# Kernel tuning notes

Measured on AMD Instinct MI355X. Metric: run time of the kernel, lower is better.

Reference implementation:

```python
import jax, jax.numpy as jnp
import numpy as np

B, MAXN, D, H, S = 64, 512, 512, 8, 32
DH = D // H          # per-head dim = 64
N = B * MAXN         # 32768 total nodes
E = 524288           # ~avg degree 16
EPS = 1e-5


def setup_inputs() -> dict:
    key = jax.random.key(0)
    ks = jax.random.split(key, 18)
    s = 0.05
    x_dense = jax.random.normal(ks[0], (B, MAXN, D), jnp.float32)
    x = jax.random.normal(ks[1], (N, D), jnp.float32)
    src = jax.random.randint(ks[2], (E,), 0, N)
    # destinations kept within the same graph as the source
    dst = (src // MAXN) * MAXN + jax.random.randint(ks[3], (E,), 0, MAXN)
    edge_index = jnp.stack([src, dst]).astype(jnp.int32)
    batch = (jnp.arange(N) // MAXN).astype(jnp.int32)  # sorted, 512 nodes/graph
    seed = jax.random.normal(ks[4], (S, 1, D), jnp.float32) * s
    # per-head GCN conv weights concatenated along output dim: [D, H*DH] == [D, D]
    Wk = jax.random.normal(ks[5], (D, D), jnp.float32) * s
    bk = jnp.zeros((D,), jnp.float32)
    Wv = jax.random.normal(ks[6], (D, D), jnp.float32) * s
    bv = jnp.zeros((D,), jnp.float32)
    q_proj_weight = jax.random.normal(ks[7], (D, D), jnp.float32) * s
    Wo = jax.random.normal(ks[8], (D, D), jnp.float32) * s
    bo = jnp.zeros((D,), jnp.float32)
    Wff = jax.random.normal(ks[9], (D, D), jnp.float32) * s
    bff = jnp.zeros((D,), jnp.float32)
    gamma_h = jnp.ones((D,), jnp.float32)
    beta_h = jnp.zeros((D,), jnp.float32)
    gamma_z = jnp.ones((D,), jnp.float32)
    beta_z = jnp.zeros((D,), jnp.float32)
    return dict(x_dense=x_dense, x=x, edge_index=edge_index, batch=batch,
                seed=seed, Wk=Wk, bk=bk, Wv=Wv, bv=bv,
                q_proj_weight=q_proj_weight, Wo=Wo, bo=bo, Wff=Wff, bff=bff,
                gamma_h=gamma_h, beta_h=beta_h, gamma_z=gamma_z, beta_z=beta_z)


def _gcn(x, W, b, src, dst):
    # PyG GCNConv with self-loops + symmetric norm; all H heads fused via W [D, H*DH]
    xw = x @ W                                   # [N, D]
    idx = jnp.arange(N)
    src_f = jnp.concatenate([src, idx])
    dst_f = jnp.concatenate([dst, idx])
    deg = jax.ops.segment_sum(jnp.ones_like(dst_f, dtype=x.dtype), dst_f, num_segments=N)
    dinv = jax.lax.rsqrt(deg)                    # deg >= 1 (self-loops)
    norm = dinv[src_f] * dinv[dst_f]             # [E+N]
    out = jax.ops.segment_sum(xw[src_f] * norm[:, None], dst_f, num_segments=N)
    return out + b


def _to_dense(feat, batch):
    # to_dense_batch for sorted batch vector; padded slots are zeros
    counts = jax.ops.segment_sum(jnp.ones((N,), jnp.int32), batch, num_segments=B)
    start = jnp.cumsum(counts) - counts
    pos = jnp.arange(N) - start[batch]
    return jnp.zeros((B, MAXN, feat.shape[-1]), feat.dtype).at[batch, pos].set(feat)


def _layernorm(x, g, b):
    m = jnp.mean(x, -1, keepdims=True)
    v = jnp.mean(jnp.square(x - m), -1, keepdims=True)
    return (x - m) * jax.lax.rsqrt(v + EPS) * g + b


def reference(x_dense, x, edge_index, batch, seed, Wk, bk, Wv, bv,
              q_proj_weight, Wo, bo, Wff, bff, gamma_h, beta_h, gamma_z, beta_z):
    src, dst = edge_index[0], edge_index[1]
    k_nodes = _gcn(x, Wk, bk, src, dst)          # [N, D] (H heads concat)
    v_nodes = _gcn(x, Wv, bv, src, dst)
    k_dense = _to_dense(k_nodes, batch)          # [B, MAXN, D]
    v_dense = _to_dense(v_nodes, batch)

    # query: seed [S,1,D] repeated over batch -> [S,B,D]; q projection (F.linear)
    query = jnp.broadcast_to(seed, (S, B, D))
    q = jnp.einsum('sbd,ed->sbe', query, q_proj_weight)
    scale = 1.0 / jnp.sqrt(jnp.float32(DH))
    qh = (q * scale).reshape(S, B, H, DH).transpose(1, 2, 0, 3)     # [B,H,S,DH]
    kh = k_dense.reshape(B, MAXN, H, DH).transpose(0, 2, 1, 3)      # [B,H,N,DH]
    vh = v_dense.reshape(B, MAXN, H, DH).transpose(0, 2, 1, 3)
    scores = jnp.einsum('bhsd,bhnd->bhsn', qh, kh)                  # [B,H,S,MAXN]
    attn = jax.nn.softmax(scores, axis=-1)                          # no padding mask (faithful)
    ctx = jnp.einsum('bhsn,bhnd->bhsd', attn, vh)                   # [B,H,S,DH]
    ctx = ctx.transpose(0, 2, 1, 3).reshape(B, S, D)                # heads concat
    attn_out = ctx @ Wo.T + bo                                      # [B,S,D]

    query_bse = jnp.broadcast_to(seed.transpose(1, 0, 2), (B, S, D))
    embed = _layernorm(query_bse + attn_out, gamma_h, beta_h)
    embed = _layernorm(embed + embed @ Wff.T + bff, gamma_z, beta_z)
    return embed
```

## Files before the change

kernel.cpp:

```cpp
#include <hip/hip_runtime.h>
#include <hip/hip_bf16.h>

#define BN   64
#define MAXN 512
#define DIM  512
#define NH   8
#define NS   32
#define NN   32768
#define NE   524288
#define MP   (2048 * 512)

typedef __hip_bfloat16 bf16;
using bf16x8 = __attribute__((ext_vector_type(8))) short;
using f32x4  = __attribute__((ext_vector_type(4))) float;

__device__ int   g_cnt[NN];
__device__ int   g_cur[NN];
__device__ int   g_off[NN + 1];
__device__ int   g_csr[NE];
__device__ float g_dinv[NN];
__device__ bf16  g_xb[NN * DIM];
__device__ bf16  g_agg[NN * DIM];
__device__ bf16  g_aggT[NN * DIM];
__device__ bf16  g_qf[256 * DIM];
__device__ bf16  g_wob[DIM * DIM];
__device__ bf16  g_wvb[DIM * DIM];
__device__ bf16  g_wvo[DIM * 8 * DIM];
__device__ float g_bvo[DIM];
__device__ bf16  g_wffT[DIM * DIM];
__device__ float g_q[NS * DIM];
__device__ bf16  g_sc[BN * 256 * MAXN];
__device__ bf16  g_cp[BN * NS * 8 * DIM];
__device__ float g_part[4 * MP];
__device__ float g_h1[BN * NS * DIM];
__device__ bf16  g_h1b[BN * NS * DIM];

__device__ inline float bf2f(unsigned short u) {
    union { unsigned int i; float f; } x; x.i = ((unsigned int)u) << 16; return x.f;
}

__device__ inline void gll16(const bf16* g, bf16* l) {
    __builtin_amdgcn_global_load_lds(
        (const __attribute__((address_space(1))) void*)g,
        (__attribute__((address_space(3))) void*)l, 16, 0, 0);
}

__global__ void k_zero() {
    int i = blockIdx.x * 256 + threadIdx.x;
    if (i < NN) { g_cnt[i] = 0; g_cur[i] = 0; }
}

__global__ __launch_bounds__(256) void k_cntprep(const int* __restrict__ dst,
                                                 const float* __restrict__ seed,
                                                 const float* __restrict__ Wq,
                                                 const float* __restrict__ Wo,
                                                 const float* __restrict__ Wv,
                                                 const float* __restrict__ Wff,
                                                 const float* __restrict__ bo,
                                                 const float* __restrict__ bv) {
    int blk = blockIdx.x;
    if (blk < 2048) {
        int e = blk * 256 + threadIdx.x;
        atomicAdd(&g_cnt[dst[e]], 1);
    } else if (blk < 2112) {
        int i = (blk - 2048) * 256 + threadIdx.x;
        int s = i >> 9, e = i & 511;
        const float* sr = seed + s * DIM;
        const float* wr = Wq + e * DIM;
        float a0 = 0.f, a1 = 0.f;
        for (int d = 0; d < DIM; d += 8) {
            float4 a = *(const float4*)(sr + d);
            float4 b = *(const float4*)(wr + d);
            float4 c = *(const float4*)(sr + d + 4);
            float4 w = *(const float4*)(wr + d + 4);
            a0 += a.x * b.x + a.y * b.y + a.z * b.z + a.w * b.w;
            a1 += c.x * w.x + c.y * w.y + c.z * w.z + c.w * w.w;
        }
        g_q[i] = (a0 + a1) * 0.125f;
    } else if (blk < 2496) {
        long t = (long)(blk - 2112) * 256 + threadIdx.x;
        const float* src; bf16* dstp; long off;
        if (t < 32768)      { src = Wo;  dstp = g_wob;  off = t; }
        else if (t < 65536) { src = Wv;  dstp = g_wvb;  off = t - 32768; }
        else                { src = Wff; dstp = g_wffT; off = t - 65536; }
        long i = off * 8;
        float4 a = *(const float4*)(src + i);
        float4 b = *(const float4*)(src + i + 4);
        float v[8] = {a.x, a.y, a.z, a.w, b.x, b.y, b.z, b.w};
        bf16x8 o;
#pragma unroll
        for (int j = 0; j < 8; j++) { bf16 q = __float2bfloat16(v[j]); o[j] = *(short*)&q; }
        *(bf16x8*)(dstp + i) = o;
    } else {
        int e = (blk - 2496) * 256 + threadIdx.x;
        const float* orow = Wo + (long)e * DIM;
        float a0 = 0.f, a1 = 0.f;
        for (int c = 0; c < DIM; c += 8) {
            float4 a = *(const float4*)(bv + c);
            float4 w = *(const float4*)(orow + c);
            float4 xx = *(const float4*)(bv + c + 4);
            float4 u = *(const float4*)(orow + c + 4);
            a0 += a.x * w.x + a.y * w.y + a.z * w.z + a.w * w.w;
            a1 += xx.x * u.x + xx.y * u.y + xx.z * u.z + xx.w * u.w;
        }
        g_bvo[e] = bo[e] + a0 + a1;
    }
}

__global__ void k_scan() {
    __shared__ int part[1024];
    int t = threadIdx.x;
    int base = t * 32;
    int loc[32]; int s = 0;
#pragma unroll
    for (int i = 0; i < 32; i++) { loc[i] = g_cnt[base + i]; s += loc[i]; }
    part[t] = s; __syncthreads();
    for (int o = 1; o < 1024; o <<= 1) {
        int v = (t >= o) ? part[t - o] : 0;
        __syncthreads();
        part[t] += v;
        __syncthreads();
    }
    int ex = (t == 0) ? 0 : part[t - 1];
#pragma unroll
    for (int i = 0; i < 32; i++) {
        g_off[base + i] = ex; ex += loc[i];
        g_dinv[base + i] = rsqrtf(1.0f + (float)loc[i]);
    }
    if (t == 1023) g_off[NN] = ex;
}

__device__ __forceinline__ void gemm128(const bf16* __restrict__ A, long lda,
                                        const bf16* __restrict__ Bt, long ldb,
                                        long row0, long col0, int kbeg, int kend,
                                        bf16 (*As)[128 * 32], bf16 (*Bs)[128 * 32],
                                        f32x4 acc[4][4]) {
    int tid = threadIdx.x;
    int lane = tid & 63, wave = tid >> 6;
    int wr = wave >> 1, wc = wave & 1;
    int fr = lane & 15, fq = lane >> 4;
    int rchunk = (fq ^ ((fr >> 1) & 3)) * 8;
    int u0 = wave * 128 + lane;
    int sr0 = u0 >> 2, sc0 = ((u0 & 3) ^ ((sr0 >> 1) & 3)) * 8;
    int u1 = u0 + 64;
    int sr1 = u1 >> 2, sc1 = ((u1 & 3) ^ ((sr1 >> 1) & 3)) * 8;

    auto stage = [&](int buf, int kt) {
        gll16(A + (row0 + sr0) * lda + kt + sc0, As[buf] + u0 * 8);
        gll16(A + (row0 + sr1) * lda + kt + sc1, As[buf] + u1 * 8);
        gll16(Bt + (col0 + sr0) * ldb + kt + sc0, Bs[buf] + u0 * 8);
        gll16(Bt + (col0 + sr1) * ldb + kt + sc1, Bs[buf] + u1 * 8);
    };

    stage(0, kbeg);
    __syncthreads();
    for (int kt = kbeg; kt < kend; kt += 32) {
        int buf = ((kt - kbeg) >> 5) & 1;
        if (kt + 32 < kend) stage(buf ^ 1, kt + 32);
        bf16x8 af[4], bfv[4];
#pragma unroll
        for (int mi = 0; mi < 4; mi++)
            af[mi] = *(const bf16x8*)(As[buf] + (wr * 64 + mi * 16 + fr) * 32 + rchunk);
#pragma unroll
        for (int ni = 0; ni < 4; ni++)
            bfv[ni] = *(const bf16x8*)(Bs[buf] + (wc * 64 + ni * 16 + fr) * 32 + rchunk);
#pragma unroll
        for (int mi = 0; mi < 4; mi++)
#pragma unroll
            for (int ni = 0; ni < 4; ni++)
                acc[mi][ni] = __builtin_amdgcn_mfma_f32_16x16x32_bf16(af[mi], bfv[ni], acc[mi][ni], 0, 0, 0);
        __syncthreads();
    }
}

#define ACC_INIT                                             \
    f32x4 acc[4][4];                                         \
    _Pragma("unroll")                                        \
    for (int i = 0; i < 4; i++)                              \
        _Pragma("unroll")                                    \
        for (int j = 0; j < 4; j++) acc[i][j] = (f32x4){0.f, 0.f, 0.f, 0.f}; \
    int lane = threadIdx.x & 63, wave = threadIdx.x >> 6;    \
    int wr = wave >> 1, wc = wave & 1;                       \
    int fr = lane & 15, fq = lane >> 4;

__global__ __launch_bounds__(256) void k_fillxb(const int* __restrict__ src,
                                                const int* __restrict__ dst,
                                                const float* __restrict__ x,
                                                const float* __restrict__ Wk) {
    __shared__ bf16 As[2][128 * 32];
    __shared__ bf16 Bs[2][128 * 32];
    int blk = blockIdx.x;
    if (blk < 2048) {
        int e = blk * 256 + threadIdx.x;
        int d = dst[e];
        int p = atomicAdd(&g_cur[d], 1);
        g_csr[g_off[d] + p] = src[e];
    } else if (blk < 10240) {
        long i = (long)(blk - 2048) * (256 * 8) + (long)threadIdx.x * 8;
        int node = (int)(i >> 9);
        float w = g_dinv[node];
        float4 a = *(const float4*)(x + i);
        float4 b = *(const float4*)(x + i + 4);
        float v[8] = {a.x, a.y, a.z, a.w, b.x, b.y, b.z, b.w};
        bf16x8 o;
#pragma unroll
        for (int j = 0; j < 8; j++) { bf16 t = __float2bfloat16(v[j] * w); o[j] = *(short*)&t; }
        *(bf16x8*)(g_xb + i) = o;
    } else if (blk < 10752) {
        int i = (blk - 10240) * 256 + threadIdx.x;
        int hs = i >> 9, d = i & 511;
        int h = hs >> 5, s = hs & 31;
        const float* qr = g_q + s * DIM + h * 64;
        const float* wr = Wk + d * DIM + h * 64;
        float a0 = 0.f, a1 = 0.f;
        for (int t2 = 0; t2 < 64; t2 += 8) {
            float4 a = *(const float4*)(qr + t2);
            float4 w = *(const float4*)(wr + t2);
            float4 c = *(const float4*)(qr + t2 + 4);
            float4 u = *(const float4*)(wr + t2 + 4);
            a0 += a.x * w.x + a.y * w.y + a.z * w.z + a.w * w.w;
            a1 += c.x * u.x + c.y * u.y + c.z * u.z + c.w * u.w;
        }
        g_qf[i] = __float2bfloat16(a0 + a1);
    } else {
        int wi = blk - 10752;
        int bx = wi & 3, by = (wi >> 2) & 3, h = wi >> 4;
        ACC_INIT
        long row0 = (long)bx * 128, col0 = (long)by * 128;
        gemm128(g_wob, DIM, g_wvb, DIM, row0, col0, h * 64, h * 64 + 64, As, Bs, acc);
#pragma unroll
        for (int mi = 0; mi < 4; mi++)
#pragma unroll
            for (int ni = 0; ni < 4; ni++) {
                long col = col0 + wc * 64 + ni * 16 + fr;
#pragma unroll
                for (int r = 0; r < 4; r++) {
                    long row = row0 + wr * 64 + mi * 16 + fq * 4 + r;
                    g_wvo[row * 4096 + h * 512 + col] = __float2bfloat16(acc[mi][ni][r]);
                }
            }
    }
}

__global__ __launch_bounds__(256) void k_gather() {
    int bid = blockIdx.x;
    int lb = (bid & 7) * 1024 + (bid >> 3);
    int wave = threadIdx.x >> 6, lane = threadIdx.x & 63;
    int node = lb * 4 + wave;

    bf16x8 sv = ((const bf16x8*)(g_xb + (long)node * DIM))[lane];
    float acc[8];
#pragma unroll
    for (int j = 0; j < 8; j++) acc[j] = bf2f((unsigned short)sv[j]);

    int e = g_off[node], e1 = g_off[node + 1];
    for (; e + 8 <= e1; e += 8) {
        bf16x8 r[8];
#pragma unroll
        for (int q = 0; q < 8; q++)
            r[q] = ((const bf16x8*)(g_xb + (long)g_csr[e + q] * DIM))[lane];
#pragma unroll
        for (int j = 0; j < 8; j++) {
            float s01 = bf2f((unsigned short)r[0][j]) + bf2f((unsigned short)r[1][j]);
            float s23 = bf2f((unsigned short)r[2][j]) + bf2f((unsigned short)r[3][j]);
            float s45 = bf2f((unsigned short)r[4][j]) + bf2f((unsigned short)r[5][j]);
            float s67 = bf2f((unsigned short)r[6][j]) + bf2f((unsigned short)r[7][j]);
            acc[j] += (s01 + s23) + (s45 + s67);
        }
    }
    for (; e < e1; e++) {
        bf16x8 r0 = ((const bf16x8*)(g_xb + (long)g_csr[e] * DIM))[lane];
#pragma unroll
        for (int j = 0; j < 8; j++) acc[j] += bf2f((unsigned short)r0[j]);
    }
    float dd = g_dinv[node];
    bf16x8 o;
#pragma unroll
    for (int j = 0; j < 8; j++) { bf16 t = __float2bfloat16(acc[j] * dd); o[j] = *(short*)&t; }
    ((bf16x8*)(g_agg + (long)node * DIM))[lane] = o;
}

__global__ __launch_bounds__(256) void k_aggsc() {
    __shared__ __align__(16) char smem[32768];
    int blk = blockIdx.x;
    if (blk < 512) {
        bf16 (*As)[128 * 32] = (bf16(*)[128 * 32])smem;
        bf16 (*Bs)[128 * 32] = (bf16(*)[128 * 32])(smem + 16384);
        int b = blk & 63, bx = (blk >> 6) & 1, by = blk >> 7;
        ACC_INIT
        long row0 = (long)bx * 128, col0 = (long)by * 128;
        gemm128(g_qf, DIM, g_agg + (long)b * (MAXN * DIM), DIM, row0, col0, 0, DIM, As, Bs, acc);
        bf16* out = g_sc + (long)b * (256 * MAXN);
#pragma unroll
        for (int mi = 0; mi < 4; mi++)
#pragma unroll
            for (int ni = 0; ni < 4; ni++) {
                long col = col0 + wc * 64 + ni * 16 + fr;
#pragma unroll
                for (int r = 0; r < 4; r++) {
                    long row = row0 + wr * 64 + mi * 16 + fq * 4 + r;
                    out[row * MAXN + col] = __float2bfloat16(acc[mi][ni][r]);
                }
            }
    } else {
        unsigned short (*L)[72] = (unsigned short(*)[72])smem;
        int id = blk - 512;
        int b = id >> 6, t = id & 63;
        int n0 = (t & 7) * 64, d0 = (t >> 3) * 64;
        int tid = threadIdx.x;
        const unsigned short* src = (const unsigned short*)g_agg + ((long)b * 512 + n0) * 512 + d0;
#pragma unroll
        for (int p = 0; p < 2; p++) {
            int r = (tid >> 3) + 32 * p, c = (tid & 7) * 8;
            *(int4*)&L[r][c] = *(const int4*)(src + (long)r * 512 + c);
        }
        __syncthreads();
        unsigned short* dst = (unsigned short*)g_aggT + ((long)b * 512 + d0) * 512 + n0;
#pragma unroll
        for (int p = 0; p < 2; p++) {
            int dr = (tid >> 3) + 32 * p, c0 = (tid & 7) * 8;
            unsigned short tmp[8];
#pragma unroll
            for (int j = 0; j < 8; j++) tmp[j] = L[c0 + j][dr];
            *(int4*)(dst + (long)dr * 512 + c0) = *(int4*)tmp;
        }
    }
}

__global__ __launch_bounds__(256) void k_soft() {
    int w = threadIdx.x >> 6, lane = threadIdx.x & 63;
    unsigned short* base = (unsigned short*)g_sc + ((long)blockIdx.x * 16 + w * 4) * MAXN;
#pragma unroll
    for (int r = 0; r < 4; r++) {
        unsigned short* row = base + (long)r * MAXN;
        float v[8]; float m = -1e30f;
#pragma unroll
        for (int k = 0; k < 8; k++) { v[k] = bf2f(row[lane + 64 * k]); m = fmaxf(m, v[k]); }
#pragma unroll
        for (int o = 32; o > 0; o >>= 1) m = fmaxf(m, __shfl_xor(m, o));
        float sum = 0.f;
#pragma unroll
        for (int k = 0; k < 8; k++) { v[k] = __expf(v[k] - m); sum += v[k]; }
#pragma unroll
        for (int o = 32; o > 0; o >>= 1) sum += __shfl_xor(sum, o);
        float inv = 1.0f / sum;
#pragma unroll
        for (int k = 0; k < 8; k++) {
            bf16 t = __float2bfloat16(v[k] * inv);
            row[lane + 64 * k] = *(unsigned short*)&t;
        }
    }
}

__global__ __launch_bounds__(256) void k_pvg() {
    __shared__ bf16 As[2][128 * 32];
    __shared__ bf16 Bs[2][128 * 32];
    int blk = blockIdx.x;
    int b = blk & 63, bx = (blk >> 6) & 1, by = (blk >> 7) & 1, dh = blk >> 8;
    ACC_INIT
    long row0 = (long)bx * 128, col0 = (long)by * 128;
    gemm128(g_sc + (long)b * (256 * MAXN), MAXN,
            g_aggT + (long)b * (DIM * MAXN) + (long)dh * (256 * MAXN), MAXN,
            row0, col0, 0, MAXN, As, Bs, acc);
#pragma unroll
    for (int mi = 0; mi < 4; mi++)
#pragma unroll
        for (int ni = 0; ni < 4; ni++) {
            long col = col0 + wc * 64 + ni * 16 + fr;
#pragma unroll
            for (int r = 0; r < 4; r++) {
                long row = row0 + wr * 64 + mi * 16 + fq * 4 + r;
                g_cp[((long)b * NS + (row & 31)) * 4096 + (row >> 5) * 512 + dh * 256 + col] =
                    __float2bfloat16(acc[mi][ni][r]);
            }
        }
}

__global__ __launch_bounds__(256) void k_vo() {
    __shared__ bf16 As[2][128 * 32];
    __shared__ bf16 Bs[2][128 * 32];
    ACC_INIT
    int z = blockIdx.z;
    long row0 = (long)blockIdx.x * 128, col0 = (long)blockIdx.y * 128;
    gemm128(g_cp, 4096, g_wvo, 4096, row0, col0, z * 1024, z * 1024 + 1024, As, Bs, acc);
    float* out = g_part + (long)z * MP;
#pragma unroll
    for (int mi = 0; mi < 4; mi++)
#pragma unroll
        for (int ni = 0; ni < 4; ni++) {
            long col = col0 + wc * 64 + ni * 16 + fr;
#pragma unroll
            for (int r = 0; r < 4; r++) {
                long row = row0 + wr * 64 + mi * 16 + fq * 4 + r;
                out[row * DIM + col] = acc[mi][ni][r];
            }
        }
}

__global__ __launch_bounds__(256) void k_ffn() {
    __shared__ bf16 As[2][128 * 32];
    __shared__ bf16 Bs[2][128 * 32];
    ACC_INIT
    int z = blockIdx.z;
    long row0 = (long)blockIdx.x * 128, col0 = (long)blockIdx.y * 128;
    gemm128(g_h1b, DIM, g_wffT, DIM, row0, col0, z * 128, z * 128 + 128, As, Bs, acc);
    float* out = g_part + (long)z * MP;
#pragma unroll
    for (int mi = 0; mi < 4; mi++)
#pragma unroll
        for (int ni = 0; ni < 4; ni++) {
            long col = col0 + wc * 64 + ni * 16 + fr;
#pragma unroll
            for (int r = 0; r < 4; r++) {
                long row = row0 + wr * 64 + mi * 16 + fq * 4 + r;
                out[row * DIM + col] = acc[mi][ni][r];
            }
        }
}

__device__ inline float blockReduceSum(float v, float* red, int tid) {
#pragma unroll
    for (int o = 32; o > 0; o >>= 1) v += __shfl_xor(v, o);
    __syncthreads();
    if ((tid & 63) == 0) red[tid >> 6] = v;
    __syncthreads();
    return red[0] + red[1] + red[2] + red[3];
}

__global__ __launch_bounds__(256) void k_ln1(const float* __restrict__ seed,
                                             const float* __restrict__ gamma,
                                             const float* __restrict__ beta) {
    __shared__ float red[4];
    int r = blockIdx.x, t = threadIdx.x;
    int s = r & 31;
    long base = (long)r * DIM;
    float v0 = seed[s * DIM + t] + g_bvo[t];
    float v1 = seed[s * DIM + 256 + t] + g_bvo[256 + t];
#pragma unroll
    for (int z = 0; z < 4; z++) {
        v0 += g_part[(long)z * MP + base + t];
        v1 += g_part[(long)z * MP + base + 256 + t];
    }
    float mean = blockReduceSum(v0 + v1, red, t) * (1.0f / DIM);
    float d0 = v0 - mean, d1 = v1 - mean;
    float var = blockReduceSum(d0 * d0 + d1 * d1, red, t) * (1.0f / DIM);
    float ri = rsqrtf(var + 1e-5f);
    float o0 = d0 * ri * gamma[t] + beta[t];
    float o1 = d1 * ri * gamma[256 + t] + beta[256 + t];
    g_h1[base + t] = o0; g_h1[base + 256 + t] = o1;
    g_h1b[base + t] = __float2bfloat16(o0);
    g_h1b[base + 256 + t] = __float2bfloat16(o1);
}

__global__ __launch_bounds__(256) void k_ln2(const float* __restrict__ gamma,
                                             const float* __restrict__ beta,
                                             const float* __restrict__ bff,
                                             float* __restrict__ out) {
    __shared__ float red[4];
    int r = blockIdx.x, t = threadIdx.x;
    long base = (long)r * DIM;
    float v0 = g_h1[base + t] + bff[t];
    float v1 = g_h1[base + 256 + t] + bff[256 + t];
#pragma unroll
    for (int z = 0; z < 4; z++) {
        v0 += g_part[(long)z * MP + base + t];
        v1 += g_part[(long)z * MP + base + 256 + t];
    }
    float mean = blockReduceSum(v0 + v1, red, t) * (1.0f / DIM);
    float d0 = v0 - mean, d1 = v1 - mean;
    float var = blockReduceSum(d0 * d0 + d1 * d1, red, t) * (1.0f / DIM);
    float ri = rsqrtf(var + 1e-5f);
    out[base + t] = d0 * ri * gamma[t] + beta[t];
    out[base + 256 + t] = d1 * ri * gamma[256 + t] + beta[256 + t];
}

extern "C" void kernel_launch(void* const* d_in, const int* in_sizes, int n_in,
                              void* d_out, int out_size, void* d_ws, size_t ws_size,
                              hipStream_t stream) {
    (void)in_sizes; (void)n_in; (void)out_size; (void)d_ws; (void)ws_size;
    const float* x    = (const float*)d_in[1];
    const int*   ei   = (const int*)d_in[2];
    const int*   esrc = ei;
    const int*   edst = ei + NE;
    const float* seed = (const float*)d_in[4];
    const float* Wk   = (const float*)d_in[5];
    const float* Wv   = (const float*)d_in[7];
    const float* bv   = (const float*)d_in[8];
    const float* Wq   = (const float*)d_in[9];
    const float* Wo   = (const float*)d_in[10];
    const float* bo   = (const float*)d_in[11];
    const float* Wff  = (const float*)d_in[12];
    const float* bff  = (const float*)d_in[13];
    const float* gh   = (const float*)d_in[14];
    const float* bh   = (const float*)d_in[15];
    const float* gz   = (const float*)d_in[16];
    const float* bz   = (const float*)d_in[17];
    float* out = (float*)d_out;

    k_zero   <<<NN / 256, 256, 0, stream>>>();
    k_cntprep<<<2498, 256, 0, stream>>>(edst, seed, Wq, Wo, Wv, Wff, bo, bv);
    k_scan   <<<1, 1024, 0, stream>>>();
    k_fillxb <<<10880, 256, 0, stream>>>(esrc, edst, x, Wk);
    k_gather <<<NN / 4, 256, 0, stream>>>();
    k_aggsc  <<<512 + BN * 64, 256, 0, stream>>>();
    k_soft   <<<1024, 256, 0, stream>>>();
    k_pvg    <<<512, 256, 0, stream>>>();
    k_vo     <<<dim3(16, 4, 4), 256, 0, stream>>>();
    k_ln1    <<<BN * NS, 256, 0, stream>>>(seed, gh, bh);
    k_ffn    <<<dim3(16, 4, 4), 256, 0, stream>>>();
    k_ln2    <<<BN * NS, 256, 0, stream>>>(gz, bz, bff, out);
}
```

Before: 253.6 us.

## Build CSR with per-block LDS histograms and column prefix instead of global atomics

Replaces the global-atomic degree count and scatter with a two-pass counting sort. Each of 256 blocks builds a full 32K-bin histogram in LDS, a column scan makes per-block prefixes, and a fill pass ranks edges with LDS atomics. This removes contended global atomics and the zeroing kernel. In exchange it adds two 16 MB ushort arrays of global traffic, 128 KB LDS per block (one block per CU), and extra launches. Weight prep is split into its own kernel.

```diff
diff --git a/kernel.cpp b/kernel.cpp
--- a/kernel.cpp
+++ b/kernel.cpp
@@ -8,16 +8,19 @@
 #define NS   32
 #define NN   32768
 #define NE   524288
+#define NBLK 256
+#define EPB  (NE / NBLK)
 #define MP   (2048 * 512)
 
 typedef __hip_bfloat16 bf16;
 using bf16x8 = __attribute__((ext_vector_type(8))) short;
 using f32x4  = __attribute__((ext_vector_type(4))) float;
 
-__device__ int   g_cnt[NN];
-__device__ int   g_cur[NN];
-__device__ int   g_off[NN + 1];
-__device__ int   g_csr[NE];
+__device__ int            g_cnt[NN];
+__device__ int            g_off[NN + 1];
+__device__ int            g_csr[NE];
+__device__ unsigned short g_hist[(long)NBLK * NN];
+__device__ unsigned short g_bpfx[(long)NBLK * NN];
 __device__ float g_dinv[NN];
 __device__ bf16  g_xb[NN * DIM];
 __device__ bf16  g_agg[NN * DIM];
@@ -45,25 +48,80 @@
         (__attribute__((address_space(3))) void*)l, 16, 0, 0);
 }
 
-__global__ void k_zero() {
-    int i = blockIdx.x * 256 + threadIdx.x;
-    if (i < NN) { g_cnt[i] = 0; g_cur[i] = 0; }
-}
-
-__global__ __launch_bounds__(256) void k_cntprep(const int* __restrict__ dst,
-                                                 const float* __restrict__ seed,
-                                                 const float* __restrict__ Wq,
-                                                 const float* __restrict__ Wo,
-                                                 const float* __restrict__ Wv,
-                                                 const float* __restrict__ Wff,
-                                                 const float* __restrict__ bo,
-                                                 const float* __restrict__ bv) {
+__global__ __launch_bounds__(512) void k_hist(const int* __restrict__ dst) {
+    __shared__ unsigned int h[NN];
+    int p = blockIdx.x, tid = threadIdx.x;
+    for (int i = tid; i < NN; i += 512) h[i] = 0;
+    __syncthreads();
+#pragma unroll
+    for (int j = 0; j < EPB / 512; j++) {
+        int e = p * EPB + j * 512 + tid;
+        atomicAdd(&h[dst[e]], 1u);
+    }
+    __syncthreads();
+    unsigned short* out = g_hist + (long)p * NN;
+    for (int i = tid; i < NN; i += 512) out[i] = (unsigned short)h[i];
+}
+
+__global__ __launch_bounds__(256) void k_colscan() {
+    int v = blockIdx.x * 256 + threadIdx.x;
+    unsigned int s = 0;
+#pragma unroll 8
+    for (int p = 0; p < NBLK; p++) {
+        unsigned int hh = g_hist[(long)p * NN + v];
+        g_bpfx[(long)p * NN + v] = (unsigned short)s;
+        s += hh;
+    }
+    g_cnt[v] = (int)s;
+    g_dinv[v] = rsqrtf(1.0f + (float)s);
+}
+
+__global__ void k_scan() {
+    __shared__ int part[1024];
+    int t = threadIdx.x;
+    int base = t * 32;
+    int loc[32]; int s = 0;
+#pragma unroll
+    for (int i = 0; i < 32; i++) { loc[i] = g_cnt[base + i]; s += loc[i]; }
+    part[t] = s; __syncthreads();
+    for (int o = 1; o < 1024; o <<= 1) {
+        int v = (t >= o) ? part[t - o] : 0;
+        __syncthreads();
+        part[t] += v;
+        __syncthreads();
+    }
+    int ex = (t == 0) ? 0 : part[t - 1];
+#pragma unroll
+    for (int i = 0; i < 32; i++) { g_off[base + i] = ex; ex += loc[i]; }
+    if (t == 1023) g_off[NN] = ex;
+}
+
+__global__ __launch_bounds__(512) void k_fillsort(const int* __restrict__ src,
+                                                  const int* __restrict__ dst) {
+    __shared__ unsigned int l[NN];
+    int p = blockIdx.x, tid = threadIdx.x;
+    const unsigned short* bp = g_bpfx + (long)p * NN;
+    for (int i = tid; i < NN; i += 512) l[i] = bp[i];
+    __syncthreads();
+#pragma unroll
+    for (int j = 0; j < EPB / 512; j++) {
+        int e = p * EPB + j * 512 + tid;
+        int v = dst[e];
+        unsigned int r = atomicAdd(&l[v], 1u);
+        g_csr[g_off[v] + r] = src[e];
+    }
+}
+
+__global__ __launch_bounds__(256) void k_prep(const float* __restrict__ seed,
+                                              const float* __restrict__ Wq,
+                                              const float* __restrict__ Wo,
+                                              const float* __restrict__ Wv,
+                                              const float* __restrict__ Wff,
+                                              const float* __restrict__ bo,
+                                              const float* __restrict__ bv) {
     int blk = blockIdx.x;
-    if (blk < 2048) {
-        int e = blk * 256 + threadIdx.x;
-        atomicAdd(&g_cnt[dst[e]], 1);
-    } else if (blk < 2112) {
-        int i = (blk - 2048) * 256 + threadIdx.x;
+    if (blk < 64) {
+        int i = blk * 256 + threadIdx.x;
         int s = i >> 9, e = i & 511;
         const float* sr = seed + s * DIM;
         const float* wr = Wq + e * DIM;
@@ -77,8 +135,8 @@
             a1 += c.x * w.x + c.y * w.y + c.z * w.z + c.w * w.w;
         }
         g_q[i] = (a0 + a1) * 0.125f;
-    } else if (blk < 2496) {
-        long t = (long)(blk - 2112) * 256 + threadIdx.x;
+    } else if (blk < 448) {
+        long t = (long)(blk - 64) * 256 + threadIdx.x;
         const float* src; bf16* dstp; long off;
         if (t < 32768)      { src = Wo;  dstp = g_wob;  off = t; }
         else if (t < 65536) { src = Wv;  dstp = g_wvb;  off = t - 32768; }
@@ -92,7 +150,7 @@
         for (int j = 0; j < 8; j++) { bf16 q = __float2bfloat16(v[j]); o[j] = *(short*)&q; }
         *(bf16x8*)(dstp + i) = o;
     } else {
-        int e = (blk - 2496) * 256 + threadIdx.x;
+        int e = (blk - 448) * 256 + threadIdx.x;
         const float* orow = Wo + (long)e * DIM;
         float a0 = 0.f, a1 = 0.f;
         for (int c = 0; c < DIM; c += 8) {
@@ -105,29 +163,6 @@
         }
         g_bvo[e] = bo[e] + a0 + a1;
     }
-}
-
-__global__ void k_scan() {
-    __shared__ int part[1024];
-    int t = threadIdx.x;
-    int base = t * 32;
-    int loc[32]; int s = 0;
-#pragma unroll
-    for (int i = 0; i < 32; i++) { loc[i] = g_cnt[base + i]; s += loc[i]; }
-    part[t] = s; __syncthreads();
-    for (int o = 1; o < 1024; o <<= 1) {
-        int v = (t >= o) ? part[t - o] : 0;
-        __syncthreads();
-        part[t] += v;
-        __syncthreads();
-    }
-    int ex = (t == 0) ? 0 : part[t - 1];
-#pragma unroll
-    for (int i = 0; i < 32; i++) {
-        g_off[base + i] = ex; ex += loc[i];
-        g_dinv[base + i] = rsqrtf(1.0f + (float)loc[i]);
-    }
-    if (t == 1023) g_off[NN] = ex;
 }
 
 __device__ __forceinline__ void gemm128(const bf16* __restrict__ A, long lda,
@@ -183,20 +218,13 @@
     int wr = wave >> 1, wc = wave & 1;                       \
     int fr = lane & 15, fq = lane >> 4;
 
-__global__ __launch_bounds__(256) void k_fillxb(const int* __restrict__ src,
-                                                const int* __restrict__ dst,
-                                                const float* __restrict__ x,
-                                                const float* __restrict__ Wk) {
+__global__ __launch_bounds__(256) void k_xbqf(const float* __restrict__ x,
+                                              const float* __restrict__ Wk) {
     __shared__ bf16 As[2][128 * 32];
     __shared__ bf16 Bs[2][128 * 32];
     int blk = blockIdx.x;
-    if (blk < 2048) {
-        int e = blk * 256 + threadIdx.x;
-        int d = dst[e];
-        int p = atomicAdd(&g_cur[d], 1);
-        g_csr[g_off[d] + p] = src[e];
-    } else if (blk < 10240) {
-        long i = (long)(blk - 2048) * (256 * 8) + (long)threadIdx.x * 8;
+    if (blk < 8192) {
+        long i = (long)blk * (256 * 8) + (long)threadIdx.x * 8;
         int node = (int)(i >> 9);
         float w = g_dinv[node];
         float4 a = *(const float4*)(x + i);
@@ -206,8 +234,8 @@
 #pragma unroll
         for (int j = 0; j < 8; j++) { bf16 t = __float2bfloat16(v[j] * w); o[j] = *(short*)&t; }
         *(bf16x8*)(g_xb + i) = o;
-    } else if (blk < 10752) {
-        int i = (blk - 10240) * 256 + threadIdx.x;
+    } else if (blk < 8704) {
+        int i = (blk - 8192) * 256 + threadIdx.x;
         int hs = i >> 9, d = i & 511;
         int h = hs >> 5, s = hs & 31;
         const float* qr = g_q + s * DIM + h * 64;
@@ -223,7 +251,7 @@
         }
         g_qf[i] = __float2bfloat16(a0 + a1);
     } else {
-        int wi = blk - 10752;
+        int wi = blk - 8704;
         int bx = wi & 3, by = (wi >> 2) & 3, h = wi >> 4;
         ACC_INIT
         long row0 = (long)bx * 128, col0 = (long)by * 128;
@@ -497,16 +525,18 @@
     const float* bz   = (const float*)d_in[17];
     float* out = (float*)d_out;
 
-    k_zero   <<<NN / 256, 256, 0, stream>>>();
-    k_cntprep<<<2498, 256, 0, stream>>>(edst, seed, Wq, Wo, Wv, Wff, bo, bv);
-    k_scan   <<<1, 1024, 0, stream>>>();
-    k_fillxb <<<10880, 256, 0, stream>>>(esrc, edst, x, Wk);
-    k_gather <<<NN / 4, 256, 0, stream>>>();
-    k_aggsc  <<<512 + BN * 64, 256, 0, stream>>>();
-    k_soft   <<<1024, 256, 0, stream>>>();
-    k_pvg    <<<512, 256, 0, stream>>>();
-    k_vo     <<<dim3(16, 4, 4), 256, 0, stream>>>();
-    k_ln1    <<<BN * NS, 256, 0, stream>>>(seed, gh, bh);
-    k_ffn    <<<dim3(16, 4, 4), 256, 0, stream>>>();
-    k_ln2    <<<BN * NS, 256, 0, stream>>>(gz, bz, bff, out);
-}
+    k_hist    <<<NBLK, 512, 0, stream>>>(edst);
+    k_colscan <<<NN / 256, 256, 0, stream>>>();
+    k_scan    <<<1, 1024, 0, stream>>>();
+    k_prep    <<<450, 256, 0, stream>>>(seed, Wq, Wo, Wv, Wff, bo, bv);
+    k_fillsort<<<NBLK, 512, 0, stream>>>(esrc, edst);
+    k_xbqf    <<<8832, 256, 0, stream>>>(x, Wk);
+    k_gather  <<<NN / 4, 256, 0, stream>>>();
+    k_aggsc   <<<512 + BN * 64, 256, 0, stream>>>();
+    k_soft    <<<1024, 256, 0, stream>>>();
+    k_pvg     <<<512, 256, 0, stream>>>();
+    k_vo      <<<dim3(16, 4, 4), 256, 0, stream>>>();
+    k_ln1     <<<BN * NS, 256, 0, stream>>>(seed, gh, bh);
+    k_ffn     <<<dim3(16, 4, 4), 256, 0, stream>>>();
+    k_ln2     <<<BN * NS, 256, 0, stream>>>(gz, bz, bff, out);
+}
```

Measured after the change: 229.4 us. 9.6% less time.

## Replace CSR sparse gather with dense per-graph adjacency GEMM on MFMA

Applied to the files above, without the earlier changes.

Instead of building a CSR (count, scan, fill) and gathering neighbour rows, the code builds a dense 512x512 per-graph adjacency of byte counts via packed atomics. It then converts it to a normalised bf16 matrix and computes aggregation as a batched GEMM against a transposed, dinv-scaled x. This removes the serial single-block scan and the irregular gather, at the cost of about 32x more FLOPs and extra memory traffic for the dense adjacency (16M bf16 plus 16M bytes). The byte counters assume fewer than 256 duplicate edges per pair, and the approach depends on edges staying within each graph.

```diff
diff --git a/kernel.cpp b/kernel.cpp
--- a/kernel.cpp
+++ b/kernel.cpp
@@ -14,12 +14,10 @@
 using bf16x8 = __attribute__((ext_vector_type(8))) short;
 using f32x4  = __attribute__((ext_vector_type(4))) float;
 
-__device__ int   g_cnt[NN];
-__device__ int   g_cur[NN];
-__device__ int   g_off[NN + 1];
-__device__ int   g_csr[NE];
+__device__ unsigned char g_adj8[(long)NN * 512];
+__device__ bf16  g_adjb[(long)NN * 512];
 __device__ float g_dinv[NN];
-__device__ bf16  g_xb[NN * DIM];
+__device__ bf16  g_xbt[(long)NN * 512];
 __device__ bf16  g_agg[NN * DIM];
 __device__ bf16  g_aggT[NN * DIM];
 __device__ bf16  g_qf[256 * DIM];
@@ -45,25 +43,40 @@
         (__attribute__((address_space(3))) void*)l, 16, 0, 0);
 }
 
-__global__ void k_zero() {
-    int i = blockIdx.x * 256 + threadIdx.x;
-    if (i < NN) { g_cnt[i] = 0; g_cur[i] = 0; }
-}
-
-__global__ __launch_bounds__(256) void k_cntprep(const int* __restrict__ dst,
-                                                 const float* __restrict__ seed,
-                                                 const float* __restrict__ Wq,
-                                                 const float* __restrict__ Wo,
-                                                 const float* __restrict__ Wv,
-                                                 const float* __restrict__ Wff,
-                                                 const float* __restrict__ bo,
-                                                 const float* __restrict__ bv) {
+__global__ __launch_bounds__(256) void k_zadj() {
+    ((int4*)g_adj8)[blockIdx.x * 256 + threadIdx.x] = make_int4(0, 0, 0, 0);
+}
+
+__global__ __launch_bounds__(256) void k_scatter(const int* __restrict__ src,
+                                                 const int* __restrict__ dst) {
+    int e = blockIdx.x * 256 + threadIdx.x;
+    int d = dst[e], s = src[e];
+    long idx = (long)d * 512 + (s & 511);
+    atomicAdd((unsigned int*)g_adj8 + (idx >> 2), 1u << ((idx & 3) * 8));
+}
+
+__global__ __launch_bounds__(256) void k_rowdeg() {
+    int node = blockIdx.x * 4 + (threadIdx.x >> 6);
+    int lane = threadIdx.x & 63;
+    const unsigned int* W = (const unsigned int*)g_adj8 + (long)node * 128;
+    unsigned int a = W[lane * 2], b = W[lane * 2 + 1];
+    int s = (int)((a & 255) + ((a >> 8) & 255) + ((a >> 16) & 255) + (a >> 24)
+                + (b & 255) + ((b >> 8) & 255) + ((b >> 16) & 255) + (b >> 24));
+#pragma unroll
+    for (int o = 32; o > 0; o >>= 1) s += __shfl_xor(s, o);
+    if (lane == 0) g_dinv[node] = rsqrtf(1.0f + (float)s);
+}
+
+__global__ __launch_bounds__(256) void k_prep(const float* __restrict__ seed,
+                                              const float* __restrict__ Wq,
+                                              const float* __restrict__ Wo,
+                                              const float* __restrict__ Wv,
+                                              const float* __restrict__ Wff,
+                                              const float* __restrict__ bo,
+                                              const float* __restrict__ bv) {
     int blk = blockIdx.x;
-    if (blk < 2048) {
-        int e = blk * 256 + threadIdx.x;
-        atomicAdd(&g_cnt[dst[e]], 1);
-    } else if (blk < 2112) {
-        int i = (blk - 2048) * 256 + threadIdx.x;
+    if (blk < 64) {
+        int i = blk * 256 + threadIdx.x;
         int s = i >> 9, e = i & 511;
         const float* sr = seed + s * DIM;
         const float* wr = Wq + e * DIM;
@@ -77,22 +90,22 @@
             a1 += c.x * w.x + c.y * w.y + c.z * w.z + c.w * w.w;
         }
         g_q[i] = (a0 + a1) * 0.125f;
-    } else if (blk < 2496) {
-        long t = (long)(blk - 2112) * 256 + threadIdx.x;
-        const float* src; bf16* dstp; long off;
-        if (t < 32768)      { src = Wo;  dstp = g_wob;  off = t; }
-        else if (t < 65536) { src = Wv;  dstp = g_wvb;  off = t - 32768; }
-        else                { src = Wff; dstp = g_wffT; off = t - 65536; }
+    } else if (blk < 448) {
+        long t = (long)(blk - 64) * 256 + threadIdx.x;
+        const float* srcp; bf16* dstp; long off;
+        if (t < 32768)      { srcp = Wo;  dstp = g_wob;  off = t; }
+        else if (t < 65536) { srcp = Wv;  dstp = g_wvb;  off = t - 32768; }
+        else                { srcp = Wff; dstp = g_wffT; off = t - 65536; }
         long i = off * 8;
-        float4 a = *(const float4*)(src + i);
-        float4 b = *(const float4*)(src + i + 4);
+        float4 a = *(const float4*)(srcp + i);
+        float4 b = *(const float4*)(srcp + i + 4);
         float v[8] = {a.x, a.y, a.z, a.w, b.x, b.y, b.z, b.w};
         bf16x8 o;
 #pragma unroll
         for (int j = 0; j < 8; j++) { bf16 q = __float2bfloat16(v[j]); o[j] = *(short*)&q; }
         *(bf16x8*)(dstp + i) = o;
     } else {
-        int e = (blk - 2496) * 256 + threadIdx.x;
+        int e = (blk - 448) * 256 + threadIdx.x;
         const float* orow = Wo + (long)e * DIM;
         float a0 = 0.f, a1 = 0.f;
         for (int c = 0; c < DIM; c += 8) {
@@ -107,27 +120,75 @@
     }
 }
 
-__global__ void k_scan() {
-    __shared__ int part[1024];
-    int t = threadIdx.x;
-    int base = t * 32;
-    int loc[32]; int s = 0;
-#pragma unroll
-    for (int i = 0; i < 32; i++) { loc[i] = g_cnt[base + i]; s += loc[i]; }
-    part[t] = s; __syncthreads();
-    for (int o = 1; o < 1024; o <<= 1) {
-        int v = (t >= o) ? part[t - o] : 0;
-        __syncthreads();
-        part[t] += v;
-        __syncthreads();
-    }
-    int ex = (t == 0) ? 0 : part[t - 1];
-#pragma unroll
-    for (int i = 0; i < 32; i++) {
-        g_off[base + i] = ex; ex += loc[i];
-        g_dinv[base + i] = rsqrtf(1.0f + (float)loc[i]);
-    }
-    if (t == 1023) g_off[NN] = ex;
+__global__ __launch_bounds__(256) void k_xbT(const float* __restrict__ x) {
+    __shared__ float L[64][65];
+    int blk = blockIdx.x;
+    int b = blk >> 6, t = blk & 63;
+    int s0 = (t & 7) * 64, f0 = (t >> 3) * 64;
+    int tid = threadIdx.x;
+#pragma unroll
+    for (int p = 0; p < 4; p++) {
+        int idx = p * 256 + tid;
+        int r = idx >> 4, c4 = (idx & 15) * 4;
+        float4 v = *(const float4*)(x + ((long)(b * 512 + s0 + r)) * 512 + f0 + c4);
+        float dv = g_dinv[b * 512 + s0 + r];
+        L[r][c4] = v.x * dv; L[r][c4 + 1] = v.y * dv;
+        L[r][c4 + 2] = v.z * dv; L[r][c4 + 3] = v.w * dv;
+    }
+    __syncthreads();
+#pragma unroll
+    for (int p = 0; p < 2; p++) {
+        int idx = p * 256 + tid;
+        int fo = idx >> 3, so8 = (idx & 7) * 8;
+        bf16x8 o;
+#pragma unroll
+        for (int j = 0; j < 8; j++) {
+            bf16 q = __float2bfloat16(L[so8 + j][fo]);
+            o[j] = *(short*)&q;
+        }
+        *(bf16x8*)(g_xbt + ((long)(b * 512 + f0 + fo)) * 512 + s0 + so8) = o;
+    }
+}
+
+__global__ __launch_bounds__(256) void k_cvtqf(const float* __restrict__ Wk) {
+    int blk = blockIdx.x;
+    if (blk < 8192) {
+        long i = ((long)blk * 256 + threadIdx.x) * 8;
+        int dst = (int)(i >> 9);
+        int s0 = (int)(i & 511);
+        const unsigned int* wp = (const unsigned int*)g_adj8 + (i >> 2);
+        unsigned int w0 = wp[0], w1 = wp[1];
+        float dv = g_dinv[dst];
+        int dl = dst & 511;
+        float c[8] = {(float)(w0 & 255), (float)((w0 >> 8) & 255),
+                      (float)((w0 >> 16) & 255), (float)(w0 >> 24),
+                      (float)(w1 & 255), (float)((w1 >> 8) & 255),
+                      (float)((w1 >> 16) & 255), (float)(w1 >> 24)};
+        bf16x8 o;
+#pragma unroll
+        for (int j = 0; j < 8; j++) {
+            float v = c[j] * dv + ((s0 + j) == dl ? dv : 0.f);
+            bf16 q = __float2bfloat16(v);
+            o[j] = *(short*)&q;
+        }
+        *(bf16x8*)(g_adjb + i) = o;
+    } else {
+        int i = (blk - 8192) * 256 + threadIdx.x;
+        int hs = i >> 9, d = i & 511;
+        int h = hs >> 5, s = hs & 31;
+        const float* qr = g_q + s * DIM + h * 64;
+        const float* wr = Wk + d * DIM + h * 64;
+        float a0 = 0.f, a1 = 0.f;
+        for (int t2 = 0; t2 < 64; t2 += 8) {
+            float4 a = *(const float4*)(qr + t2);
+            float4 w = *(const float4*)(wr + t2);
+            float4 c = *(const float4*)(qr + t2 + 4);
+            float4 u = *(const float4*)(wr + t2 + 4);
+            a0 += a.x * w.x + a.y * w.y + a.z * w.z + a.w * w.w;
+            a1 += c.x * u.x + c.y * u.y + c.z * u.z + c.w * u.w;
+        }
+        g_qf[i] = __float2bfloat16(a0 + a1);
+    }
 }
 
 __device__ __forceinline__ void gemm128(const bf16* __restrict__ A, long lda,
@@ -183,47 +244,31 @@
     int wr = wave >> 1, wc = wave & 1;                       \
     int fr = lane & 15, fq = lane >> 4;
 
-__global__ __launch_bounds__(256) void k_fillxb(const int* __restrict__ src,
-                                                const int* __restrict__ dst,
-                                                const float* __restrict__ x,
-                                                const float* __restrict__ Wk) {
+__global__ __launch_bounds__(256) void k_adjgemm() {
     __shared__ bf16 As[2][128 * 32];
     __shared__ bf16 Bs[2][128 * 32];
     int blk = blockIdx.x;
-    if (blk < 2048) {
-        int e = blk * 256 + threadIdx.x;
-        int d = dst[e];
-        int p = atomicAdd(&g_cur[d], 1);
-        g_csr[g_off[d] + p] = src[e];
-    } else if (blk < 10240) {
-        long i = (long)(blk - 2048) * (256 * 8) + (long)threadIdx.x * 8;
-        int node = (int)(i >> 9);
-        float w = g_dinv[node];
-        float4 a = *(const float4*)(x + i);
-        float4 b = *(const float4*)(x + i + 4);
-        float v[8] = {a.x, a.y, a.z, a.w, b.x, b.y, b.z, b.w};
-        bf16x8 o;
-#pragma unroll
-        for (int j = 0; j < 8; j++) { bf16 t = __float2bfloat16(v[j] * w); o[j] = *(short*)&t; }
-        *(bf16x8*)(g_xb + i) = o;
-    } else if (blk < 10752) {
-        int i = (blk - 10240) * 256 + threadIdx.x;
-        int hs = i >> 9, d = i & 511;
-        int h = hs >> 5, s = hs & 31;
-        const float* qr = g_q + s * DIM + h * 64;
-        const float* wr = Wk + d * DIM + h * 64;
-        float a0 = 0.f, a1 = 0.f;
-        for (int t2 = 0; t2 < 64; t2 += 8) {
-            float4 a = *(const float4*)(qr + t2);
-            float4 w = *(const float4*)(wr + t2);
-            float4 c = *(const float4*)(qr + t2 + 4);
-            float4 u = *(const float4*)(wr + t2 + 4);
-            a0 += a.x * w.x + a.y * w.y + a.z * w.z + a.w * w.w;
-            a1 += c.x * u.x + c.y * u.y + c.z * u.z + c.w * u.w;
-        }
-        g_qf[i] = __float2bfloat16(a0 + a1);
+    if (blk < 1024) {
+        int b = blk & 63, bx = (blk >> 6) & 3, by = blk >> 8;
+        ACC_INIT
+        long row0 = (long)bx * 128, col0 = (long)by * 128;
+        const bf16* A  = g_adjb + (long)b * 512 * 512;
+        const bf16* Bt = g_xbt  + (long)b * 512 * 512;
+        gemm128(A, 512, Bt, 512, row0, col0, 0, 512, As, Bs, acc);
+        bf16* out = g_agg + (long)b * 512 * 512;
+#pragma unroll
+        for (int mi = 0; mi < 4; mi++)
+#pragma unroll
+            for (int ni = 0; ni < 4; ni++) {
+                long col = col0 + wc * 64 + ni * 16 + fr;
+#pragma unroll
+                for (int r = 0; r < 4; r++) {
+                    long row = row0 + wr * 64 + mi * 16 + fq * 4 + r;
+                    out[row * 512 + col] = __float2bfloat16(acc[mi][ni][r]);
+                }
+            }
     } else {
-        int wi = blk - 10752;
+        int wi = blk - 1024;
         int bx = wi & 3, by = (wi >> 2) & 3, h = wi >> 4;
         ACC_INIT
         long row0 = (long)bx * 128, col0 = (long)by * 128;
@@ -240,44 +285,6 @@
                 }
             }
     }
-}
-
-__global__ __launch_bounds__(256) void k_gather() {
-    int bid = blockIdx.x;
-    int lb = (bid & 7) * 1024 + (bid >> 3);
-    int wave = threadIdx.x >> 6, lane = threadIdx.x & 63;
-    int node = lb * 4 + wave;
-
-    bf16x8 sv = ((const bf16x8*)(g_xb + (long)node * DIM))[lane];
-    float acc[8];
-#pragma unroll
-    for (int j = 0; j < 8; j++) acc[j] = bf2f((unsigned short)sv[j]);
-
-    int e = g_off[node], e1 = g_off[node + 1];
-    for (; e + 8 <= e1; e += 8) {
-        bf16x8 r[8];
-#pragma unroll
-        for (int q = 0; q < 8; q++)
-            r[q] = ((const bf16x8*)(g_xb + (long)g_csr[e + q] * DIM))[lane];
-#pragma unroll
-        for (int j = 0; j < 8; j++) {
-            float s01 = bf2f((unsigned short)r[0][j]) + bf2f((unsigned short)r[1][j]);
-            float s23 = bf2f((unsigned short)r[2][j]) + bf2f((unsigned short)r[3][j]);
-            float s45 = bf2f((unsigned short)r[4][j]) + bf2f((unsigned short)r[5][j]);
-            float s67 = bf2f((unsigned short)r[6][j]) + bf2f((unsigned short)r[7][j]);
-            acc[j] += (s01 + s23) + (s45 + s67);
-        }
-    }
-    for (; e < e1; e++) {
-        bf16x8 r0 = ((const bf16x8*)(g_xb + (long)g_csr[e] * DIM))[lane];
-#pragma unroll
-        for (int j = 0; j < 8; j++) acc[j] += bf2f((unsigned short)r0[j]);
-    }
-    float dd = g_dinv[node];
-    bf16x8 o;
-#pragma unroll
-    for (int j = 0; j < 8; j++) { bf16 t = __float2bfloat16(acc[j] * dd); o[j] = *(short*)&t; }
-    ((bf16x8*)(g_agg + (long)node * DIM))[lane] = o;
 }
 
 __global__ __launch_bounds__(256) void k_aggsc() {
@@ -497,11 +504,13 @@
     const float* bz   = (const float*)d_in[17];
     float* out = (float*)d_out;
 
-    k_zero   <<<NN / 256, 256, 0, stream>>>();
-    k_cntprep<<<2498, 256, 0, stream>>>(edst, seed, Wq, Wo, Wv, Wff, bo, bv);
-    k_scan   <<<1, 1024, 0, stream>>>();
-    k_fillxb <<<10880, 256, 0, stream>>>(esrc, edst, x, Wk);
-    k_gather <<<NN / 4, 256, 0, stream>>>();
+    k_zadj   <<<4096, 256, 0, stream>>>();
+    k_prep   <<<450, 256, 0, stream>>>(seed, Wq, Wo, Wv, Wff, bo, bv);
+    k_scatter<<<NE / 256, 256, 0, stream>>>(esrc, edst);
+    k_rowdeg <<<NN / 4, 256, 0, stream>>>();
+    k_xbT    <<<4096, 256, 0, stream>>>(x);
+    k_cvtqf  <<<8704, 256, 0, stream>>>(Wk);
+    k_adjgemm<<<1152, 256, 0, stream>>>();
     k_aggsc  <<<512 + BN * 64, 256, 0, stream>>>();
     k_soft   <<<1024, 256, 0, stream>>>();
     k_pvg    <<<512, 256, 0, stream>>>();
```

New measurement: 264.8 us. +4.4%, slower.
